# Kernel tuning notes

Hardware: AMD Instinct MI355X
Metric: run time of the kernel (lower is better)

Reference implementation:

```python
import jax, jax.numpy as jnp
import numpy as np

COST_PROB = 1.0
COST_HEAT = 1.0


def _cost_blocks(prob, label, heat, gt):
    """Diagonal blocks of the matcher cost: C[b] = cost_heat*L1cdist(heat[b], gt[b]) + cost_prob*(1 - prob[b][:, label[b]]).
    Only these blocks are consumed by the per-batch linear_sum_assignment in the original module.
    Returns [bs, nq, ngt]."""
    bs, nq, _ = prob.shape
    ngt = gt.shape[1]
    # L1 cdist per batch: [bs, nq, ngt]
    cost_h = jnp.abs(heat[:, :, None, :] - gt[:, None, :, :]).sum(-1)
    idx = jnp.broadcast_to(label[:, None, :], (bs, nq, ngt))
    cls_prob = jnp.take_along_axis(prob, idx, axis=2)  # prob[b, q, label[b, g]]
    cost_p = 1.0 - cls_prob
    return COST_HEAT * cost_h + COST_PROB * cost_p


def _lsap(cost):
    """Exact rectangular LSAP (Jonker-Volgenant shortest augmenting path, same algorithm as
    scipy.optimize.linear_sum_assignment). cost is [n, m] with n <= m (here n=ngt, m=nq).
    Returns (row_ind, col_ind) matching scipy's output on the transposed [m, n] matrix:
    row_ind = matched query indices (sorted ascending), col_ind = corresponding gt indices."""
    n, m = cost.shape
    INF = jnp.array(jnp.inf, cost.dtype)

    def solve_row(cur_row, carry):
        u, v, col4row, row4col = carry

        # --- Dijkstra search for shortest augmenting path from cur_row ---
        def dij_cond(st):
            return st[6] < 0

        def dij_body(st):
            i, minVal, SR, SC, shortest, path, sink = st
            SR = SR.at[i].set(True)
            lowest = minVal + cost[i] - u[i] - v  # reduced costs along row i, shape [m]
            upd = (~SC) & (lowest < shortest)
            shortest = jnp.where(upd, lowest, shortest)
            path = jnp.where(upd, i, path)
            masked = jnp.where(SC, INF, shortest)
            j = jnp.argmin(masked).astype(jnp.int32)
            minVal = masked[j]
            SC = SC.at[j].set(True)
            r = row4col[j]
            sink = jnp.where(r < 0, j, jnp.int32(-1))
            i = jnp.where(r < 0, i, r)
            return (i, minVal, SR, SC, shortest, path, sink)

        init = (jnp.int32(cur_row), jnp.array(0.0, cost.dtype),
                jnp.zeros((n,), bool), jnp.zeros((m,), bool),
                jnp.full((m,), INF), jnp.zeros((m,), jnp.int32), jnp.int32(-1))
        _, minVal, SR, SC, shortest, path, sink = jax.lax.while_loop(dij_cond, dij_body, init)

        # --- dual updates ---
        rows = jnp.arange(n)
        u = u.at[cur_row].add(minVal)
        u = u + jnp.where(SR & (rows != cur_row), minVal - shortest[col4row], jnp.array(0.0, cost.dtype))
        v = v - jnp.where(SC, minVal - shortest, jnp.array(0.0, cost.dtype))

        # --- augment along the alternating path back from sink ---
        def aug_cond(st):
            return ~st[3]

        def aug_body(st):
            j, c4r, r4c, _ = st
            i = path[j]
            r4c = r4c.at[j].set(i)
            prev = c4r[i]
            c4r = c4r.at[i].set(j)
            return (prev, c4r, r4c, i == jnp.int32(cur_row))

        _, col4row, row4col, _ = jax.lax.while_loop(
            aug_cond, aug_body, (sink, col4row, row4col, jnp.array(False)))
        return (u, v, col4row, row4col)

    carry0 = (jnp.zeros((n,), cost.dtype), jnp.zeros((m,), cost.dtype),
              jnp.full((n,), -1, jnp.int32), jnp.full((m,), -1, jnp.int32))
    _, _, col4row, _ = jax.lax.fori_loop(0, n, solve_row, carry0)
    order = jnp.argsort(col4row)          # gt indices ordered by matched query index
    return col4row[order], order.astype(jnp.int32)


def setup_inputs() -> dict:
    key = jax.random.key(0)
    k1, k2, k3, k4 = jax.random.split(key, 4)
    bs, nq, ngt, D, ncls = 16, 64, 32, 4096, 33
    prob = jax.random.uniform(k1, (bs, nq, ncls), jnp.float32)
    label = jax.random.randint(k2, (bs, ngt), 0, ncls, jnp.int32)
    heat = jax.random.uniform(k3, (bs, nq, D), jnp.float32)
    gt = jax.random.uniform(k4, (bs, ngt, D), jnp.float32)
    return {"prob": prob, "label": label, "heat": heat, "gt": gt}


def reference(prob, label, heat, gt):
    C = _cost_blocks(prob, label, heat, gt)           # [bs, nq, ngt]
    rows, cols = jax.vmap(_lsap)(jnp.swapaxes(C, 1, 2))  # solve on [ngt, nq] per sample
    return rows, cols                                  # each [bs, ngt]: (query idx sorted, gt idx)
```

## Files before the change

### kernel.cpp

```cpp
#include <hip/hip_runtime.h>
#include <hip/hip_bf16.h>

#define BS   16
#define NQ   64
#define NGT  32
#define DIM  4096
#define NCLS 33

#define QT      4
#define NCHUNK  4
#define CHUNK   (DIM / NCHUNK)

__global__ __launch_bounds__(256) void cost_kernel(
    const float* __restrict__ heat, const float* __restrict__ gt,
    float* __restrict__ Cp)
{
    __shared__ float hrow[QT][CHUNK];
    const int bid  = blockIdx.x;
    const int b    = bid & 15;
    const int rest = bid >> 4;
    const int qt   = rest & (NQ / QT - 1);
    const int c    = rest >> 4;
    const int q0   = qt * QT;

    const float* hbase = heat + ((size_t)(b * NQ + q0)) * DIM + c * CHUNK;
    for (int i = threadIdx.x; i < QT * CHUNK / 4; i += 256) {
        int r = i >> 8;
        int k = i & 255;
        ((float4*)hrow[r])[k] = ((const float4*)(hbase + (size_t)r * DIM))[k];
    }
    __syncthreads();

    const int wave = threadIdx.x >> 6;
    const int lane = threadIdx.x & 63;
    const int g0 = wave * 8;
    const float* gbase = gt + ((size_t)(b * NGT + g0)) * DIM + c * CHUNK;

    float acc[8][QT];
    #pragma unroll
    for (int g = 0; g < 8; ++g)
        #pragma unroll
        for (int q = 0; q < QT; ++q) acc[g][q] = 0.f;

    for (int i = lane; i < CHUNK / 4; i += 64) {
        float4 hv[QT];
        #pragma unroll
        for (int q = 0; q < QT; ++q) hv[q] = ((float4*)hrow[q])[i];
        #pragma unroll
        for (int g = 0; g < 8; ++g) {
            float4 gv = ((const float4*)(gbase + (size_t)g * DIM))[i];
            #pragma unroll
            for (int q = 0; q < QT; ++q) {
                acc[g][q] += fabsf(hv[q].x - gv.x) + fabsf(hv[q].y - gv.y) +
                             fabsf(hv[q].z - gv.z) + fabsf(hv[q].w - gv.w);
            }
        }
    }

    float r[32];
    #pragma unroll
    for (int k = 0; k < 32; ++k) r[k] = acc[k >> 2][k & 3];
    #pragma unroll
    for (int n = 32, m = 1; n > 1; n >>= 1, m <<= 1) {
        #pragma unroll
        for (int k = 0; k < 32; ++k) {
            if (k < n / 2) {
                float a  = r[2 * k], bb = r[2 * k + 1];
                bool  hi = (lane & m) != 0;
                float keep = hi ? bb : a;
                float send = hi ? a : bb;
                r[k] = keep + __shfl_xor(send, m);
            }
        }
    }
    float tot = r[0] + __shfl_xor(r[0], 32);
    if (lane < 32) {
        int gl = lane >> 2, ql = lane & 3;
        Cp[((size_t)((c * BS + b) * NQ + (q0 + ql))) * NGT + (g0 + gl)] = tot;
    }
}

__device__ __forceinline__ float dppmin(float x, const int ctrl) {
    int t;
    switch (ctrl) {
        case 0xB1:  t = __builtin_amdgcn_update_dpp(0, __float_as_int(x), 0xB1,  0xf, 0xf, true); break;
        case 0x4E:  t = __builtin_amdgcn_update_dpp(0, __float_as_int(x), 0x4E,  0xf, 0xf, true); break;
        case 0x141: t = __builtin_amdgcn_update_dpp(0, __float_as_int(x), 0x141, 0xf, 0xf, true); break;
        default:    t = __builtin_amdgcn_update_dpp(0, __float_as_int(x), 0x140, 0xf, 0xf, true); break;
    }
    return fminf(x, __int_as_float(t));
}
__device__ __forceinline__ float rdlane_f(float x, int l) {
    return __int_as_float(__builtin_amdgcn_readlane(__float_as_int(x), l));
}

__global__ __launch_bounds__(64) void lsap_kernel(
    const float* __restrict__ Cp, const float* __restrict__ prob,
    const int* __restrict__ label, int* __restrict__ out)
{
    __shared__ float cost[NGT * NQ];
    const int b = blockIdx.x;
    const int lane = threadIdx.x;

    for (int idx = lane; idx < NQ * NGT; idx += 64) {
        int q = idx >> 5;
        int g = idx & 31;
        float ch = 0.f;
        #pragma unroll
        for (int c = 0; c < NCHUNK; ++c)
            ch += Cp[((size_t)((c * BS + b) * NQ + q)) * NGT + g];
        int lb = label[b * NGT + g];
        float cpr = 1.0f - prob[((size_t)b * NQ + q) * NCLS + lb];
        cost[g * 64 + q] = ch + cpr;
    }
    __syncthreads();

    const float INF = __builtin_inff();

    float v = 0.f;
    float u_reg = 0.f;
    int c4r = -1;
    int r4c = -1;

    for (int cur = 0; cur < NGT; ++cur) {
        unsigned SRmask = 0;
        float shortest = INF;
        int pathv = 0;
        bool SC = false;
        float minVal = 0.f;
        int i = cur;
        int sink = -1;

        while (sink < 0) {
            SRmask |= (1u << i);
            float ci = cost[(i << 6) + lane];
            float ui = rdlane_f(u_reg, i);
            float lowest = minVal + ci - ui - v;
            if (!SC && lowest < shortest) { shortest = lowest; pathv = i; }
            float masked = SC ? INF : shortest;
            float x = masked;
            x = dppmin(x, 0xB1);
            x = dppmin(x, 0x4E);
            x = dppmin(x, 0x141);
            x = dppmin(x, 0x140);
            float mv = rdlane_f(x, 0);
            mv = fminf(mv, rdlane_f(x, 16));
            mv = fminf(mv, rdlane_f(x, 32));
            mv = fminf(mv, rdlane_f(x, 48));
            unsigned long long ball = __ballot(masked == mv);
            int j = __ffsll(ball) - 1;
            minVal = mv;
            if (lane == j) SC = true;
            int r = __builtin_amdgcn_readlane(r4c, j);
            if (r < 0) sink = j;
            else       i = r;
        }

        if (lane == cur) u_reg += minVal;
        {
            float shc = __shfl(shortest, c4r & 63);
            bool rowupd = (lane < NGT) && (lane != cur) && ((SRmask >> lane) & 1u);
            if (rowupd) u_reg += minVal - shc;
        }
        if (SC) v -= minVal - shortest;

        int j = sink;
        while (true) {
            int ii = __builtin_amdgcn_readlane(pathv, j);
            if (lane == j) r4c = ii;
            int prev = __builtin_amdgcn_readlane(c4r, ii);
            if (lane == ii) c4r = j;
            if (ii == cur) break;
            j = prev;
        }
    }

    int c = c4r;
    int rank = 0;
    for (int t = 0; t < NGT; ++t) {
        int ct = __shfl(c4r, t);
        rank += (ct < c) ? 1 : 0;
    }
    if (lane < NGT) {
        out[b * NGT + rank] = c;
        out[BS * NGT + b * NGT + rank] = lane;
    }
}

extern "C" void kernel_launch(void* const* d_in, const int* in_sizes, int n_in,
                              void* d_out, int out_size, void* d_ws, size_t ws_size,
                              hipStream_t stream) {
    const float* prob  = (const float*)d_in[0];
    const int*   label = (const int*)d_in[1];
    const float* heat  = (const float*)d_in[2];
    const float* gt    = (const float*)d_in[3];
    int* out = (int*)d_out;
    float* Cp = (float*)d_ws;

    cost_kernel<<<dim3(BS * (NQ / QT) * NCHUNK), dim3(256), 0, stream>>>(heat, gt, Cp);
    lsap_kernel<<<dim3(BS), dim3(64), 0, stream>>>(Cp, prob, label, out);
}
```

Measured before the change: 41.47 us.

## Fuse cost and LSAP kernels via last-block-done atomic counter per batch

Merges the cost computation and the assignment solver into one kernel. Each block bumps a per-batch atomic counter, and the last block to finish a batch runs the LSAP solve in its first wave, reusing shared memory for the cost matrix. The partial-cost layout is changed so the four chunk partials sit together and can be read with one float4. The change also fully unrolls the inner distance loop and raises wave priority during the solve. This removes the second kernel launch and lets batches solve as soon as their data is ready, but it adds a memset launch and atomics with fences.

```diff
diff --git a/kernel.cpp b/kernel.cpp
--- a/kernel.cpp
+++ b/kernel.cpp
@@ -10,12 +10,29 @@
 #define QT      4
 #define NCHUNK  4
 #define CHUNK   (DIM / NCHUNK)
-
-__global__ __launch_bounds__(256) void cost_kernel(
+#define BLOCKS_PER_BATCH ((NQ / QT) * NCHUNK)
+
+__device__ __forceinline__ float dppmin(float x, const int ctrl) {
+    int t;
+    switch (ctrl) {
+        case 0xB1:  t = __builtin_amdgcn_update_dpp(0, __float_as_int(x), 0xB1,  0xf, 0xf, true); break;
+        case 0x4E:  t = __builtin_amdgcn_update_dpp(0, __float_as_int(x), 0x4E,  0xf, 0xf, true); break;
+        case 0x141: t = __builtin_amdgcn_update_dpp(0, __float_as_int(x), 0x141, 0xf, 0xf, true); break;
+        default:    t = __builtin_amdgcn_update_dpp(0, __float_as_int(x), 0x140, 0xf, 0xf, true); break;
+    }
+    return fminf(x, __int_as_float(t));
+}
+__device__ __forceinline__ float rdlane_f(float x, int l) {
+    return __int_as_float(__builtin_amdgcn_readlane(__float_as_int(x), l));
+}
+
+__global__ __launch_bounds__(256) void fused_kernel(
+    const float* __restrict__ prob, const int* __restrict__ label,
     const float* __restrict__ heat, const float* __restrict__ gt,
-    float* __restrict__ Cp)
+    float* __restrict__ Cp, int* __restrict__ flags, int* __restrict__ out)
 {
     __shared__ float hrow[QT][CHUNK];
+    __shared__ int is_last_s;
     const int bid  = blockIdx.x;
     const int b    = bid & 15;
     const int rest = bid >> 4;
@@ -42,7 +59,9 @@
         #pragma unroll
         for (int q = 0; q < QT; ++q) acc[g][q] = 0.f;
 
-    for (int i = lane; i < CHUNK / 4; i += 64) {
+    #pragma unroll
+    for (int i0 = 0; i0 < CHUNK / 4; i0 += 64) {
+        const int i = i0 + lane;
         float4 hv[QT];
         #pragma unroll
         for (int q = 0; q < QT; ++q) hv[q] = ((float4*)hrow[q])[i];
@@ -76,47 +95,33 @@
     float tot = r[0] + __shfl_xor(r[0], 32);
     if (lane < 32) {
         int gl = lane >> 2, ql = lane & 3;
-        Cp[((size_t)((c * BS + b) * NQ + (q0 + ql))) * NGT + (g0 + gl)] = tot;
-    }
-}
-
-__device__ __forceinline__ float dppmin(float x, const int ctrl) {
-    int t;
-    switch (ctrl) {
-        case 0xB1:  t = __builtin_amdgcn_update_dpp(0, __float_as_int(x), 0xB1,  0xf, 0xf, true); break;
-        case 0x4E:  t = __builtin_amdgcn_update_dpp(0, __float_as_int(x), 0x4E,  0xf, 0xf, true); break;
-        case 0x141: t = __builtin_amdgcn_update_dpp(0, __float_as_int(x), 0x141, 0xf, 0xf, true); break;
-        default:    t = __builtin_amdgcn_update_dpp(0, __float_as_int(x), 0x140, 0xf, 0xf, true); break;
-    }
-    return fminf(x, __int_as_float(t));
-}
-__device__ __forceinline__ float rdlane_f(float x, int l) {
-    return __int_as_float(__builtin_amdgcn_readlane(__float_as_int(x), l));
-}
-
-__global__ __launch_bounds__(64) void lsap_kernel(
-    const float* __restrict__ Cp, const float* __restrict__ prob,
-    const int* __restrict__ label, int* __restrict__ out)
-{
-    __shared__ float cost[NGT * NQ];
-    const int b = blockIdx.x;
-    const int lane = threadIdx.x;
-
+        Cp[(((size_t)(b * NQ + (q0 + ql))) * NGT + (g0 + gl)) * NCHUNK + c] = tot;
+    }
+
+    __syncthreads();
+    if (threadIdx.x == 0) {
+        __threadfence();
+        int old = atomicAdd(&flags[b], 1);
+        is_last_s = (old == BLOCKS_PER_BATCH - 1);
+    }
+    __syncthreads();
+    if (!is_last_s || threadIdx.x >= 64) return;
+
+    __threadfence();
+    __builtin_amdgcn_s_setprio(1);
+
+    float* cost = &hrow[0][0];
     for (int idx = lane; idx < NQ * NGT; idx += 64) {
         int q = idx >> 5;
         int g = idx & 31;
-        float ch = 0.f;
-        #pragma unroll
-        for (int c = 0; c < NCHUNK; ++c)
-            ch += Cp[((size_t)((c * BS + b) * NQ + q)) * NGT + g];
+        float4 v4 = *(const float4*)&Cp[(((size_t)(b * NQ + q)) * NGT + g) * NCHUNK];
         int lb = label[b * NGT + g];
-        float cpr = 1.0f - prob[((size_t)b * NQ + q) * NCLS + lb];
-        cost[g * 64 + q] = ch + cpr;
-    }
-    __syncthreads();
+        float cpr = 1.0f - prob[((size_t)(b * NQ + q)) * NCLS + lb];
+        cost[g * 64 + q] = ((v4.x + v4.y) + (v4.z + v4.w)) + cpr;
+    }
+    asm volatile("s_waitcnt lgkmcnt(0)" ::: "memory");
 
     const float INF = __builtin_inff();
-
     float v = 0.f;
     float u_reg = 0.f;
     int c4r = -1;
@@ -151,9 +156,9 @@
             int j = __ffsll(ball) - 1;
             minVal = mv;
             if (lane == j) SC = true;
-            int r = __builtin_amdgcn_readlane(r4c, j);
-            if (r < 0) sink = j;
-            else       i = r;
+            int rr = __builtin_amdgcn_readlane(r4c, j);
+            if (rr < 0) sink = j;
+            else        i = rr;
         }
 
         if (lane == cur) u_reg += minVal;
@@ -174,15 +179,16 @@
             j = prev;
         }
     }
-
-    int c = c4r;
+    __builtin_amdgcn_s_setprio(0);
+
+    int cc = c4r;
     int rank = 0;
     for (int t = 0; t < NGT; ++t) {
         int ct = __shfl(c4r, t);
-        rank += (ct < c) ? 1 : 0;
+        rank += (ct < cc) ? 1 : 0;
     }
     if (lane < NGT) {
-        out[b * NGT + rank] = c;
+        out[b * NGT + rank] = cc;
         out[BS * NGT + b * NGT + rank] = lane;
     }
 }
@@ -196,7 +202,9 @@
     const float* gt    = (const float*)d_in[3];
     int* out = (int*)d_out;
     float* Cp = (float*)d_ws;
-
-    cost_kernel<<<dim3(BS * (NQ / QT) * NCHUNK), dim3(256), 0, stream>>>(heat, gt, Cp);
-    lsap_kernel<<<dim3(BS), dim3(64), 0, stream>>>(Cp, prob, label, out);
-}
+    int* flags = (int*)((char*)d_ws + (size_t)BS * NQ * NGT * NCHUNK * 4);
+
+    hipMemsetAsync(flags, 0, BS * sizeof(int), stream);
+    fused_kernel<<<dim3(BS * (NQ / QT) * NCHUNK), dim3(256), 0, stream>>>(
+        prob, label, heat, gt, Cp, flags, out);
+}
```

Result: slower. 63.10 us (+52.2%).

## Use 8x8 query/chunk tiling, chunk-contiguous partials, and 256-thread cost assembly

Applied to the files above, without the earlier changes.

The cost kernel now handles 8 queries per block over 8 D-chunks instead of 4x4, so each gt load is reused across more queries. The butterfly reduction is widened to 64 values, which lets every lane store a result. Partial sums are stored with the chunk index innermost, so the LSAP kernel can read all of them with two float4 loads. The LSAP kernel uses 256 threads to build the cost matrix and then keeps one wave for the solver. The tradeoff is higher register pressure from the 64-entry accumulator and smaller per-chunk work in each block.

```diff
diff --git a/kernel.cpp b/kernel.cpp
--- a/kernel.cpp
+++ b/kernel.cpp
@@ -7,8 +7,8 @@
 #define DIM  4096
 #define NCLS 33
 
-#define QT      4
-#define NCHUNK  4
+#define QT      8
+#define NCHUNK  8
 #define CHUNK   (DIM / NCHUNK)
 
 __global__ __launch_bounds__(256) void cost_kernel(
@@ -20,13 +20,13 @@
     const int b    = bid & 15;
     const int rest = bid >> 4;
     const int qt   = rest & (NQ / QT - 1);
-    const int c    = rest >> 4;
+    const int c    = rest >> 3;
     const int q0   = qt * QT;
 
     const float* hbase = heat + ((size_t)(b * NQ + q0)) * DIM + c * CHUNK;
     for (int i = threadIdx.x; i < QT * CHUNK / 4; i += 256) {
-        int r = i >> 8;
-        int k = i & 255;
+        int r = i >> 7;
+        int k = i & 127;
         ((float4*)hrow[r])[k] = ((const float4*)(hbase + (size_t)r * DIM))[k];
     }
     __syncthreads();
@@ -57,11 +57,11 @@
         }
     }
 
-    float r[32];
+    float r[64];
     #pragma unroll
-    for (int k = 0; k < 32; ++k) r[k] = acc[k >> 2][k & 3];
+    for (int k = 0; k < 64; ++k) r[k] = acc[k >> 3][k & 7];
     #pragma unroll
-    for (int n = 32, m = 1; n > 1; n >>= 1, m <<= 1) {
+    for (int n = 64, m = 1; n > 1; n >>= 1, m <<= 1) {
         #pragma unroll
         for (int k = 0; k < 32; ++k) {
             if (k < n / 2) {
@@ -73,10 +73,9 @@
             }
         }
     }
-    float tot = r[0] + __shfl_xor(r[0], 32);
-    if (lane < 32) {
-        int gl = lane >> 2, ql = lane & 3;
-        Cp[((size_t)((c * BS + b) * NQ + (q0 + ql))) * NGT + (g0 + gl)] = tot;
+    {
+        int gl = lane >> 3, ql = lane & 7;
+        Cp[(((size_t)(b * NQ + (q0 + ql))) * NGT + (g0 + gl)) * NCHUNK + c] = r[0];
     }
 }
 
@@ -94,29 +93,31 @@
     return __int_as_float(__builtin_amdgcn_readlane(__float_as_int(x), l));
 }
 
-__global__ __launch_bounds__(64) void lsap_kernel(
+__global__ __launch_bounds__(256) void lsap_kernel(
     const float* __restrict__ Cp, const float* __restrict__ prob,
     const int* __restrict__ label, int* __restrict__ out)
 {
     __shared__ float cost[NGT * NQ];
     const int b = blockIdx.x;
-    const int lane = threadIdx.x;
-
-    for (int idx = lane; idx < NQ * NGT; idx += 64) {
-        int q = idx >> 5;
-        int g = idx & 31;
-        float ch = 0.f;
-        #pragma unroll
-        for (int c = 0; c < NCHUNK; ++c)
-            ch += Cp[((size_t)((c * BS + b) * NQ + q)) * NGT + g];
+    const int tid = threadIdx.x;
+
+    for (int idx = tid; idx < NQ * NGT; idx += 256) {
+        int q = idx & 63;
+        int g = idx >> 6;
+        const float* p = &Cp[(((size_t)(b * NQ + q)) * NGT + g) * NCHUNK];
+        float4 v4a = *(const float4*)p;
+        float4 v4b = *(const float4*)(p + 4);
         int lb = label[b * NGT + g];
-        float cpr = 1.0f - prob[((size_t)b * NQ + q) * NCLS + lb];
-        cost[g * 64 + q] = ch + cpr;
+        float cpr = 1.0f - prob[((size_t)(b * NQ + q)) * NCLS + lb];
+        float s = ((v4a.x + v4a.y) + (v4a.z + v4a.w)) +
+                  ((v4b.x + v4b.y) + (v4b.z + v4b.w));
+        cost[g * 64 + q] = s + cpr;
     }
     __syncthreads();
+    if (tid >= 64) return;
+    const int lane = tid;
 
     const float INF = __builtin_inff();
-
     float v = 0.f;
     float u_reg = 0.f;
     int c4r = -1;
@@ -151,9 +152,9 @@
             int j = __ffsll(ball) - 1;
             minVal = mv;
             if (lane == j) SC = true;
-            int r = __builtin_amdgcn_readlane(r4c, j);
-            if (r < 0) sink = j;
-            else       i = r;
+            int rr = __builtin_amdgcn_readlane(r4c, j);
+            if (rr < 0) sink = j;
+            else        i = rr;
         }
 
         if (lane == cur) u_reg += minVal;
@@ -175,14 +176,14 @@
         }
     }
 
-    int c = c4r;
+    int cc = c4r;
     int rank = 0;
     for (int t = 0; t < NGT; ++t) {
         int ct = __shfl(c4r, t);
-        rank += (ct < c) ? 1 : 0;
+        rank += (ct < cc) ? 1 : 0;
     }
     if (lane < NGT) {
-        out[b * NGT + rank] = c;
+        out[b * NGT + rank] = cc;
         out[BS * NGT + b * NGT + rank] = lane;
     }
 }
@@ -198,5 +199,5 @@
     float* Cp = (float*)d_ws;
 
     cost_kernel<<<dim3(BS * (NQ / QT) * NCHUNK), dim3(256), 0, stream>>>(heat, gt, Cp);
-    lsap_kernel<<<dim3(BS), dim3(64), 0, stream>>>(Cp, prob, label, out);
-}
+    lsap_kernel<<<dim3(BS), dim3(256), 0, stream>>>(Cp, prob, label, out);
+}
```

Measured after the change: 41.49 us. About the same (+0.0%).
